# Kernel optimization log

Measured on AMD Instinct MI355X. Metric: run time of the kernel, lower is better.

The kernel has to match this reference:

```python
import jax, jax.numpy as jnp
import numpy as np
from jax import lax

HEADS = 8  # num_heads; also must equal cols of the input

def _conv_same(x, W, b):
    # x: (N, C_in, H, W), W: (C_out, C_in, kh, kw) -- Conv2d with padding='same'
    y = lax.conv_general_dilated(x, W, (1, 1), 'SAME',
                                 dimension_numbers=('NCHW', 'OIHW', 'NCHW'))
    return y + b[None, :, None, None]

def setup_inputs() -> dict:
    key = jax.random.key(0)
    ks = jax.random.split(key, 11)
    B, S, D, R, C = 4, 8, 512, 32, 8  # cols C == num_heads (required by the reshape)
    f = 3
    inp = {
        'q': jax.random.normal(ks[0], (B, S, D, R, C), jnp.float32),
        'k': jax.random.normal(ks[1], (B, S, D, R, C), jnp.float32),
        'v': jax.random.normal(ks[2], (B, S, D, R, C), jnp.float32),
        'Wq': jax.random.normal(ks[3], (D, D, f, f), jnp.float32) * 0.02,
        'bq': jnp.zeros((D,), jnp.float32),
        'Wk': jax.random.normal(ks[4], (D, D, f, f), jnp.float32) * 0.02,
        'bk': jnp.zeros((D,), jnp.float32),
        'Wv': jax.random.normal(ks[5], (D, D, f, f), jnp.float32) * 0.02,
        'bv': jnp.zeros((D,), jnp.float32),
        'Wo': jax.random.normal(ks[6], (D, D, f, f), jnp.float32) * 0.02,
        'bo': jnp.zeros((D,), jnp.float32),
    }
    return inp

def reference(q, k, v, Wq, bq, Wk, bk, Wv, bv, Wo, bo):
    B, S, D, R, C = q.shape
    H = HEADS
    dep = C // H  # = 1 with C == H (attention 'depth' per the original view math)

    def proj_split(x, W, b):
        y = _conv_same(x.reshape(B * S, D, R, C), W, b)          # (N, D, R, C)
        y = y.reshape(1, H, B * S, D, R, C // H)                  # raw view as in torch
        return y.transpose(0, 2, 3, 4, 1, 5)                      # (1, N, D, R, H, dep)

    q6 = proj_split(q, Wq, bq)
    k6 = proj_split(k, Wk, bk)
    v6 = proj_split(v, Wv, bv)

    # vectorized form of the per-step loop: dot over (rows, H, dep), softmax over keys
    scores = jnp.einsum('bnqrhd,bnkrhd->bnqk', q6, k6) / jnp.sqrt(jnp.float32(dep))
    attn = jax.nn.softmax(scores, axis=-1)                        # (1, N, D, D)
    out = jnp.einsum('bnqk,bnkrhd->bnqrhd', attn, v6)             # (1, N, D, R, H, dep)

    sa = out.reshape(B, S, R, H, D).transpose(0, 4, 1, 2, 3)      # (B, D, S, R, H)
    y = _conv_same(sa.reshape(B, D, S, R * H), Wo, bo)            # channels = d_model
    y = y.reshape(B, D, S, R, H)
    return y, attn
```

## Files before the change

### kernel.cpp

```cpp
#include <hip/hip_runtime.h>


typedef __attribute__((ext_vector_type(8))) short short8;
typedef __attribute__((ext_vector_type(8))) _Float16 half8;
typedef __attribute__((ext_vector_type(4))) float f32x4;
typedef __attribute__((ext_vector_type(4))) short short4v;

#define MFMA16F(a, b, c) __builtin_amdgcn_mfma_f32_16x16x32_f16((a), (b), (c), 0, 0, 0)

__device__ __forceinline__ void gl_lds16(const void* g, void* l) {
    __builtin_amdgcn_global_load_lds(
        (const __attribute__((address_space(1))) unsigned int*)g,
        (__attribute__((address_space(3))) unsigned int*)l, 16, 0, 0);
}
__device__ __forceinline__ unsigned short f2h(float f) {
    _Float16 h = (_Float16)f;
    return __builtin_bit_cast(unsigned short, h);
}
__device__ __forceinline__ float h2f(unsigned short u) {
    return (float)__builtin_bit_cast(_Float16, u);
}

__global__ __launch_bounds__(256) void k_prep_fused(
        const float* __restrict__ q, const float* __restrict__ k,
        const float* __restrict__ v,
        const float* __restrict__ Wq, const float* __restrict__ Wk,
        const float* __restrict__ Wv, const float* __restrict__ Wo,
        unsigned short* __restrict__ Wqh, unsigned short* __restrict__ Wkh,
        unsigned short* __restrict__ Wvh, unsigned short* __restrict__ Woh,
        unsigned short* __restrict__ Xqh, unsigned short* __restrict__ Xkh,
        unsigned short* __restrict__ Xvh) {
    __shared__ __align__(16) unsigned int U[8192];
    const int b = blockIdx.x;
    const int tid = threadIdx.x;
    if (b < 1536) {
        const int cig = b & 15, n = (b >> 4) & 31, z = b >> 9;
        const float* X = z == 0 ? q : z == 1 ? k : v;
        unsigned short* Xh = z == 0 ? Xqh : z == 1 ? Xkh : Xvh;
#pragma unroll
        for (int it = 0; it < 8; ++it) {
            int ci_l = it * 4 + (tid >> 6);
            int pos = (tid & 63) * 4;
            const float4 rd =
                *(const float4*)&X[(size_t)(n * 512 + cig * 32 + ci_l) * 256 + pos];
            uint4 u;
            u.x = f2h(rd.x);
            u.y = f2h(rd.y);
            u.z = f2h(rd.z);
            u.w = f2h(rd.w);
            *(uint4*)&U[ci_l * 256 + pos] = u;
        }
        __syncthreads();
#pragma unroll
        for (int it = 0; it < 4; ++it) {
            int pos = it * 64 + (tid >> 2);
            int ci8 = (tid & 3) * 8;
            short8 h8;
#pragma unroll
            for (int j = 0; j < 8; ++j)
                h8[j] = (short)(U[(ci8 + j) * 256 + pos] & 0xffffu);
            int yy = (pos >> 3) + 1, xx = (pos & 7) + 1;
            size_t o = (size_t)((n * 34 + yy) * 10 + xx) * 512 + cig * 32 + ci8;
            *(short8*)&Xh[o] = h8;
        }
    } else if (b < 3584) {
        const int bl = b - 1536;
        const int co = bl & 511, z = bl >> 9;
        const float* W = z == 0 ? Wq : z == 1 ? Wk : z == 2 ? Wv : Wo;
        unsigned short* Wh = z == 0 ? Wqh : z == 1 ? Wkh : z == 2 ? Wvh : Woh;
        const float* Wc = W + co * 4608;
#pragma unroll
        for (int it = 0; it < 9; ++it) {
            int p = it * 256 + tid;
            float2 rd = *(const float2*)&Wc[p * 2];
            int e0 = p * 2;
            int ci0 = e0 / 9, t0 = e0 - ci0 * 9;
            U[t0 * 512 + ci0] = f2h(rd.x);
            int e1 = e0 + 1;
            int ci1 = e1 / 9, t1 = e1 - ci1 * 9;
            U[t1 * 512 + ci1] = f2h(rd.y);
        }
        __syncthreads();
        unsigned short* Whc = Wh + co * 4608;
#pragma unroll
        for (int it = 0; it < 18; ++it) {
            int j = it * 256 + tid;
            Whc[j] = (unsigned short)U[j];
        }
    } else {
        const int w = tid >> 6, l = tid & 63;
        int job = (b - 3584) * 4 + w;
        int a = job / 2688;
        int r = job - a * 2688;
        int n = r / 84;
        int ii = r - n * 84;
        unsigned short* arr = a == 0 ? Xqh : a == 1 ? Xkh : Xvh;
        int cell;
        if (ii < 11)      cell = ii;
        else if (ii < 73) { int j = ii - 11; cell = 19 + (j >> 1) * 10 + (j & 1); }
        else              cell = 329 + (ii - 73);
        short8 z8 = {0, 0, 0, 0, 0, 0, 0, 0};
        *(short8*)&arr[(size_t)(n * 340 + cell) * 512 + l * 8] = z8;
    }
}

__global__ __launch_bounds__(256) void k_conv_qkv_all(
        const unsigned short* __restrict__ Xqh, const unsigned short* __restrict__ Xkh,
        const unsigned short* __restrict__ Xvh,
        const unsigned short* __restrict__ Wqh_, const unsigned short* __restrict__ Wkh_,
        const unsigned short* __restrict__ Wvh_,
        const float* __restrict__ bq, const float* __restrict__ bk,
        const float* __restrict__ bv,
        unsigned short* __restrict__ Qh, unsigned short* __restrict__ Ql,
        unsigned short* __restrict__ Kh,
        unsigned short* __restrict__ Vt) {
    __shared__ __align__(16) short Ah[8192], Bh[8192];
    const int z = blockIdx.z;
    const unsigned short* Xh = z == 0 ? Xqh : z == 1 ? Xkh : Xvh;
    const unsigned short* Wh = z == 0 ? Wqh_ : z == 1 ? Wkh_ : Wvh_;
    const float* bias = z == 0 ? bq : z == 1 ? bk : bv;

    const int tid = threadIdx.x;
    const int w = tid >> 6, l = tid & 63;
    const int n   = blockIdx.x >> 1;
    const int p0  = (blockIdx.x & 1) * 128;
    const int co0 = blockIdx.y * 128;
    const int lm = l & 15, lq = l >> 4;
    const int r8 = l >> 3, c8 = (l & 7) ^ (l >> 3);

    int arow[4], brow[4];
#pragma unroll
    for (int j = 0; j < 4; ++j) {
        int rt = w * 32 + j * 8 + r8;
        int px = p0 + rt;
        int y = px >> 3, x = px & 7;
        arow[j] = ((n * 34 + y + 1) * 10 + (x + 1)) * 512 + c8 * 8;
        brow[j] = (co0 + rt) * 4608 + c8 * 8;
    }
    const int ldsW = w * 4096;

    int aoff[4][2], boff[4][2];
#pragma unroll
    for (int mi = 0; mi < 4; ++mi) {
        int row = (w & 1) * 64 + mi * 16 + lm;
#pragma unroll
        for (int ks = 0; ks < 2; ++ks)
            aoff[mi][ks] = row * 64 + ((((ks << 2) | lq) ^ (row & 7)) * 8);
    }
#pragma unroll
    for (int ni = 0; ni < 4; ++ni) {
        int row = (w >> 1) * 64 + ni * 16 + lm;
#pragma unroll
        for (int ks = 0; ks < 2; ++ks)
            boff[ni][ks] = row * 64 + ((((ks << 2) | lq) ^ (row & 7)) * 8);
    }

    f32x4 acc[4][4];
#pragma unroll
    for (int ni = 0; ni < 4; ++ni) {
        float b = bias[co0 + (w >> 1) * 64 + ni * 16 + lm];
#pragma unroll
        for (int mi = 0; mi < 4; ++mi) acc[mi][ni] = (f32x4){b, b, b, b};
    }

    for (int tap = 0; tap < 9; ++tap) {
        const int tapoff = ((tap / 3 - 1) * 10 + (tap % 3 - 1)) * 512;
        const int wb = tap * 512;
        for (int ci0 = 0; ci0 < 512; ci0 += 64) {
#pragma unroll
            for (int j = 0; j < 4; ++j)
                gl_lds16(Xh + arow[j] + tapoff + ci0, (char*)Ah + ldsW + j * 1024);
#pragma unroll
            for (int j = 0; j < 4; ++j)
                gl_lds16(Wh + brow[j] + wb + ci0, (char*)Bh + ldsW + j * 1024);
            __syncthreads();
            __builtin_amdgcn_s_setprio(1);
#pragma unroll
            for (int ks = 0; ks < 2; ++ks) {
                half8 ah[4], bh[4];
#pragma unroll
                for (int mi = 0; mi < 4; ++mi)
                    ah[mi] = *(const half8*)&Ah[aoff[mi][ks]];
#pragma unroll
                for (int ni = 0; ni < 4; ++ni)
                    bh[ni] = *(const half8*)&Bh[boff[ni][ks]];
#pragma unroll
                for (int mi = 0; mi < 4; ++mi)
#pragma unroll
                    for (int ni = 0; ni < 4; ++ni)
                        acc[mi][ni] = MFMA16F(ah[mi], bh[ni], acc[mi][ni]);
            }
            __builtin_amdgcn_s_setprio(0);
            __syncthreads();
        }
    }

    const int hh = n >> 2, nl = n & 3;
    const int pxbase = p0 + (w & 1) * 64 + lq * 4;
    const int x0q = pxbase & 7;
#pragma unroll
    for (int mi = 0; mi < 4; ++mi) {
        int px = pxbase + mi * 16;
        int y = px >> 3;
#pragma unroll
        for (int ni = 0; ni < 4; ++ni) {
            int co = co0 + (w >> 1) * 64 + ni * 16 + lm;
            int nn = nl * 8 + (co >> 6);
            int dd = (co & 63) * 8 + (y >> 2);
            int t0 = hh * 32 + (y & 3) * 8 + x0q;
            if (z == 0) {
                short4v hv, lv;
#pragma unroll
                for (int r = 0; r < 4; ++r) {
                    float xv = acc[mi][ni][r];
                    unsigned short hb = f2h(xv);
                    hv[r] = (short)hb;
                    lv[r] = (short)f2h(xv - h2f(hb));
                }
                int base = (nn * 512 + dd) * 256 + t0;
                *(short4v*)&Qh[base] = hv;
                *(short4v*)&Ql[base] = lv;
            } else if (z == 1) {
                short4v hv;
#pragma unroll
                for (int r = 0; r < 4; ++r) hv[r] = (short)f2h(acc[mi][ni][r]);
                *(short4v*)&Kh[(nn * 512 + dd) * 256 + t0] = hv;
            } else {
#pragma unroll
                for (int r = 0; r < 4; ++r)
                    Vt[(nn * 256 + t0 + r) * 512 + dd] = f2h(acc[mi][ni][r]);
            }
        }
    }
}

__global__ __launch_bounds__(256) void k_scores_mfma(
        const unsigned short* __restrict__ Qh, const unsigned short* __restrict__ Ql,
        const unsigned short* __restrict__ Kh,
        float* __restrict__ Sc) {
    __shared__ __align__(16) short Ah[8192], Al[8192], Bh[8192];
    const int tid = threadIdx.x;
    const int w = tid >> 6, l = tid & 63;
    const int q0 = blockIdx.x * 128, k0 = blockIdx.y * 128, nn = blockIdx.z;
    const int lm = l & 15, lq = l >> 4;
    const int r8 = l >> 3, c8 = (l & 7) ^ (l >> 3);

    int arow[4], brow[4];
#pragma unroll
    for (int j = 0; j < 4; ++j) {
        int rr = w * 32 + j * 8 + r8;
        arow[j] = (nn * 512 + q0 + rr) * 256 + c8 * 8;
        brow[j] = (nn * 512 + k0 + rr) * 256 + c8 * 8;
    }
    const int ldsW = w * 4096;

    int aoff[4][2], boff[4][2];
#pragma unroll
    for (int mi = 0; mi < 4; ++mi) {
        int row = (w & 1) * 64 + mi * 16 + lm;
#pragma unroll
        for (int ks = 0; ks < 2; ++ks)
            aoff[mi][ks] = row * 64 + ((((ks << 2) | lq) ^ (row & 7)) * 8);
    }
#pragma unroll
    for (int ni = 0; ni < 4; ++ni) {
        int row = (w >> 1) * 64 + ni * 16 + lm;
#pragma unroll
        for (int ks = 0; ks < 2; ++ks)
            boff[ni][ks] = row * 64 + ((((ks << 2) | lq) ^ (row & 7)) * 8);
    }

    f32x4 acc[4][4];
#pragma unroll
    for (int mi = 0; mi < 4; ++mi)
#pragma unroll
        for (int ni = 0; ni < 4; ++ni) acc[mi][ni] = (f32x4){0.f, 0.f, 0.f, 0.f};

    for (int t0 = 0; t0 < 256; t0 += 64) {
#pragma unroll
        for (int j = 0; j < 4; ++j)
            gl_lds16(Qh + arow[j] + t0, (char*)Ah + ldsW + j * 1024);
#pragma unroll
        for (int j = 0; j < 4; ++j)
            gl_lds16(Ql + arow[j] + t0, (char*)Al + ldsW + j * 1024);
#pragma unroll
        for (int j = 0; j < 4; ++j)
            gl_lds16(Kh + brow[j] + t0, (char*)Bh + ldsW + j * 1024);
        __syncthreads();
#pragma unroll
        for (int ks = 0; ks < 2; ++ks) {
            half8 ah[4], bh[4];
#pragma unroll
            for (int mi = 0; mi < 4; ++mi) ah[mi] = *(const half8*)&Ah[aoff[mi][ks]];
#pragma unroll
            for (int ni = 0; ni < 4; ++ni) bh[ni] = *(const half8*)&Bh[boff[ni][ks]];
#pragma unroll
            for (int mi = 0; mi < 4; ++mi)
#pragma unroll
                for (int ni = 0; ni < 4; ++ni)
                    acc[mi][ni] = MFMA16F(ah[mi], bh[ni], acc[mi][ni]);
            half8 alv[4];
#pragma unroll
            for (int mi = 0; mi < 4; ++mi) alv[mi] = *(const half8*)&Al[aoff[mi][ks]];
#pragma unroll
            for (int mi = 0; mi < 4; ++mi)
#pragma unroll
                for (int ni = 0; ni < 4; ++ni)
                    acc[mi][ni] = MFMA16F(alv[mi], bh[ni], acc[mi][ni]);
        }
        __syncthreads();
    }

    float* C = Sc + nn * 262144;
#pragma unroll
    for (int mi = 0; mi < 4; ++mi) {
        int qb = q0 + (w & 1) * 64 + lq * 4 + mi * 16;
#pragma unroll
        for (int ni = 0; ni < 4; ++ni) {
            int col = k0 + (w >> 1) * 64 + ni * 16 + lm;
#pragma unroll
            for (int r = 0; r < 4; ++r)
                C[(qb + r) * 512 + col] = acc[mi][ni][r];
        }
    }
}

__global__ __launch_bounds__(256) void k_softmax(float* __restrict__ Sc,
                                                 unsigned short* __restrict__ Ph,
                                                 unsigned int* __restrict__ Spz) {
    unsigned zi = blockIdx.x * 256 + threadIdx.x;
    if (zi < 2641920u) Spz[zi] = 0u;
    __shared__ float red[8];
    float* p = Sc + (size_t)blockIdx.x * 512;
    unsigned short* ph = Ph + (size_t)blockIdx.x * 512;
    const int tid = threadIdx.x;
    float x0 = p[tid], x1 = p[tid + 256];
    float m = fmaxf(x0, x1);
#pragma unroll
    for (int off = 32; off; off >>= 1) m = fmaxf(m, __shfl_xor(m, off));
    if ((tid & 63) == 0) red[tid >> 6] = m;
    __syncthreads();
    m = fmaxf(fmaxf(red[0], red[1]), fmaxf(red[2], red[3]));
    float e0 = __expf(x0 - m), e1 = __expf(x1 - m);
    float s = e0 + e1;
#pragma unroll
    for (int off = 32; off; off >>= 1) s += __shfl_xor(s, off);
    if ((tid & 63) == 0) red[4 + (tid >> 6)] = s;
    __syncthreads();
    s = red[4] + red[5] + red[6] + red[7];
    float inv = 1.0f / s;
    float p0 = e0 * inv, p1 = e1 * inv;
    p[tid] = p0;
    p[tid + 256] = p1;
    ph[tid] = f2h(p0);
    ph[tid + 256] = f2h(p1);
}

__global__ __launch_bounds__(256) void k_pv_mfma(
        const unsigned short* __restrict__ Ph, const unsigned short* __restrict__ Vt,
        unsigned short* __restrict__ Sp) {
    __shared__ __align__(16) short Ah[16384], Bh[8192];
    const int tid = threadIdx.x;
    const int w = tid >> 6, l = tid & 63;
    const int q0 = blockIdx.x * 128, t0 = blockIdx.y * 64, nn = blockIdx.z;
    const int lm = l & 15, lq = l >> 4;
    const int r4 = l >> 4, c16 = l & 15;

    int arow[8], brow[4];
#pragma unroll
    for (int j = 0; j < 8; ++j) {
        int rt = w * 32 + j * 4 + r4;
        arow[j] = (nn * 512 + q0 + rt) * 512 + ((c16 ^ (rt & 15)) * 8);
    }
#pragma unroll
    for (int j = 0; j < 4; ++j) {
        int rt = w * 16 + j * 4 + r4;
        brow[j] = (nn * 256 + t0 + rt) * 512 + ((c16 ^ (rt & 15)) * 8);
    }
    const int ldsA = w * 8192, ldsB = w * 4096;

    int aoff[4][4], boff[2][4];
#pragma unroll
    for (int mi = 0; mi < 4; ++mi) {
        int row = (w & 1) * 64 + mi * 16 + lm;
#pragma unroll
        for (int ks = 0; ks < 4; ++ks)
            aoff[mi][ks] = row * 128 + ((((ks << 2) | lq) ^ (row & 15)) * 8);
    }
#pragma unroll
    for (int ni = 0; ni < 2; ++ni) {
        int row = (w >> 1) * 32 + ni * 16 + lm;
#pragma unroll
        for (int ks = 0; ks < 4; ++ks)
            boff[ni][ks] = row * 128 + ((((ks << 2) | lq) ^ (row & 15)) * 8);
    }

    f32x4 acc[4][2];
#pragma unroll
    for (int mi = 0; mi < 4; ++mi)
#pragma unroll
        for (int ni = 0; ni < 2; ++ni) acc[mi][ni] = (f32x4){0.f, 0.f, 0.f, 0.f};

    for (int kc = 0; kc < 512; kc += 128) {
#pragma unroll
        for (int j = 0; j < 8; ++j)
            gl_lds16(Ph + arow[j] + kc, (char*)Ah + ldsA + j * 1024);
#pragma unroll
        for (int j = 0; j < 4; ++j)
            gl_lds16(Vt + brow[j] + kc, (char*)Bh + ldsB + j * 1024);
        __syncthreads();
#pragma unroll
        for (int ks = 0; ks < 4; ++ks) {
            half8 a[4], b[2];
#pragma unroll
            for (int mi = 0; mi < 4; ++mi) a[mi] = *(const half8*)&Ah[aoff[mi][ks]];
#pragma unroll
            for (int ni = 0; ni < 2; ++ni) b[ni] = *(const half8*)&Bh[boff[ni][ks]];
#pragma unroll
            for (int mi = 0; mi < 4; ++mi)
#pragma unroll
                for (int ni = 0; ni < 2; ++ni)
                    acc[mi][ni] = MFMA16F(a[mi], b[ni], acc[mi][ni]);
        }
        __syncthreads();
    }

    const int b2 = nn >> 3, s2 = nn & 7;
#pragma unroll
    for (int mi = 0; mi < 4; ++mi) {
        int qb = q0 + (w & 1) * 64 + lq * 4 + mi * 16;
#pragma unroll
        for (int ni = 0; ni < 2; ++ni) {
            int tc = t0 + (w >> 1) * 32 + ni * 16 + lm;
            int d2base = (tc & 31) * 8 + (tc >> 5);
#pragma unroll
            for (int r = 0; r < 4; ++r) {
                int qp = qb + r;
                int ww = (qp >> 4) * 8 + ((qp >> 1) & 7);
                int d2 = (qp & 1) * 256 + d2base;
                Sp[((b2 * 10 + s2 + 1) * 258 + ww + 1) * 512 + d2] =
                    f2h(acc[mi][ni][r]);
            }
        }
    }
}

__global__ __launch_bounds__(256) void k_conv_o_mfma(
        const unsigned short* __restrict__ Sp, const unsigned short* __restrict__ Wh,
        const float* __restrict__ bias, float* __restrict__ Y) {
    __shared__ __align__(16) short Ah[16384], Bh[8192];
    const int tid = threadIdx.x;
    const int w = tid >> 6, l = tid & 63;
    const int n   = blockIdx.x >> 4;
    const int yy  = (blockIdx.x >> 1) & 7;
    const int x0  = (blockIdx.x & 1) * 128;
    const int co0 = blockIdx.y * 64;
    const int lm = l & 15, lq = l >> 4;
    const int r4 = l >> 4, c16 = l & 15;

    int arow[8], brow[4];
#pragma unroll
    for (int j = 0; j < 8; ++j) {
        int rt = w * 32 + j * 4 + r4;
        arow[j] = ((n * 10 + yy + 1) * 258 + (x0 + rt + 1)) * 512
                  + ((c16 ^ (rt & 15)) * 8);
    }
#pragma unroll
    for (int j = 0; j < 4; ++j) {
        int rt = w * 16 + j * 4 + r4;
        brow[j] = (co0 + rt) * 4608 + ((c16 ^ (rt & 15)) * 8);
    }
    const int ldsA = w * 8192, ldsB = w * 4096;

    int aoff[4][4], boff[2][4];
#pragma unroll
    for (int mi = 0; mi < 4; ++mi) {
        int row = (w & 1) * 64 + mi * 16 + lm;
#pragma unroll
        for (int ks = 0; ks < 4; ++ks)
            aoff[mi][ks] = row * 128 + ((((ks << 2) | lq) ^ (row & 15)) * 8);
    }
#pragma unroll
    for (int ni = 0; ni < 2; ++ni) {
        int row = (w >> 1) * 32 + ni * 16 + lm;
#pragma unroll
        for (int ks = 0; ks < 4; ++ks)
            boff[ni][ks] = row * 128 + ((((ks << 2) | lq) ^ (row & 15)) * 8);
    }

    f32x4 acc[4][2];
#pragma unroll
    for (int ni = 0; ni < 2; ++ni) {
        float b = bias[co0 + (w >> 1) * 32 + ni * 16 + lm];
#pragma unroll
        for (int mi = 0; mi < 4; ++mi) acc[mi][ni] = (f32x4){b, b, b, b};
    }

    for (int tap = 0; tap < 9; ++tap) {
        const int tapoff = ((tap / 3 - 1) * 258 + (tap % 3 - 1)) * 512;
        const int wb = tap * 512;
        for (int ci0 = 0; ci0 < 512; ci0 += 128) {
#pragma unroll
            for (int j = 0; j < 8; ++j)
                gl_lds16(Sp + arow[j] + tapoff + ci0, (char*)Ah + ldsA + j * 1024);
#pragma unroll
            for (int j = 0; j < 4; ++j)
                gl_lds16(Wh + brow[j] + wb + ci0, (char*)Bh + ldsB + j * 1024);
            __syncthreads();
#pragma unroll
            for (int ks = 0; ks < 4; ++ks) {
                half8 a[4], b[2];
#pragma unroll
                for (int mi = 0; mi < 4; ++mi)
                    a[mi] = *(const half8*)&Ah[aoff[mi][ks]];
#pragma unroll
                for (int ni = 0; ni < 2; ++ni)
                    b[ni] = *(const half8*)&Bh[boff[ni][ks]];
#pragma unroll
                for (int mi = 0; mi < 4; ++mi)
#pragma unroll
                    for (int ni = 0; ni < 2; ++ni)
                        acc[mi][ni] = MFMA16F(a[mi], b[ni], acc[mi][ni]);
            }
            __syncthreads();
        }
    }

#pragma unroll
    for (int mi = 0; mi < 4; ++mi) {
        int px = x0 + (w & 1) * 64 + lq * 4 + mi * 16;
#pragma unroll
        for (int ni = 0; ni < 2; ++ni) {
            int co = co0 + (w >> 1) * 32 + ni * 16 + lm;
            *(f32x4*)&Y[n * 1048576 + co * 2048 + yy * 256 + px] = acc[mi][ni];
        }
    }
}

extern "C" void kernel_launch(void* const* d_in, const int* in_sizes, int n_in,
                              void* d_out, int out_size, void* d_ws, size_t ws_size,
                              hipStream_t stream) {
    const float* q  = (const float*)d_in[0];
    const float* k  = (const float*)d_in[1];
    const float* v  = (const float*)d_in[2];
    const float* Wq = (const float*)d_in[3];
    const float* bq = (const float*)d_in[4];
    const float* Wk = (const float*)d_in[5];
    const float* bk = (const float*)d_in[6];
    const float* Wv = (const float*)d_in[7];
    const float* bv = (const float*)d_in[8];
    const float* Wo = (const float*)d_in[9];
    const float* bo = (const float*)d_in[10];

    unsigned short* W0  = (unsigned short*)d_ws;
    unsigned short* Wqh = W0;
    unsigned short* Wkh = W0 + 2359296;
    unsigned short* Wvh = W0 + 4718592;
    unsigned short* Xvh = W0 + 7077888;
    unsigned short* Woh = W0 + 18219008;
    unsigned short* Qh  = W0 + 20578304;
    unsigned short* Ql  = W0 + 24772608;
    unsigned short* Kh  = W0 + 28966912;
    unsigned short* Vt  = W0 + 33161216;
    unsigned short* Ph = W0;
    unsigned short* Sp = W0 + 20578304;

    float* y_out = (float*)d_out;
    float* attn  = y_out + 4194304;
    unsigned short* Xqh = (unsigned short*)d_out;
    unsigned short* Xkh = (unsigned short*)attn;

    k_prep_fused<<<5600, 256, 0, stream>>>(q, k, v, Wq, Wk, Wv, Wo,
                                           Wqh, Wkh, Wvh, Woh,
                                           Xqh, Xkh, Xvh);
    k_conv_qkv_all<<<dim3(64, 4, 3), 256, 0, stream>>>(
        Xqh, Xkh, Xvh, Wqh, Wkh, Wvh,
        bq, bk, bv, Qh, Ql, Kh, Vt);
    k_scores_mfma<<<dim3(4, 4, 32), 256, 0, stream>>>(Qh, Ql, Kh, attn);
    k_softmax<<<16384, 256, 0, stream>>>(attn, Ph, (unsigned int*)Sp);
    k_pv_mfma<<<dim3(4, 4, 32), 256, 0, stream>>>(Ph, Vt, Sp);
    k_conv_o_mfma<<<dim3(64, 8), 256, 0, stream>>>(Sp, Woh, bo, y_out);
}
```

Measured before the change: 376.9 us.

## Drop Q low-half split precision, widen scores K-tile, warp-per-row softmax

Removes the hi/lo fp16 split of Q, so the scores GEMM runs a single fp16 MFMA pass and no longer writes or loads the Ql buffer. The scores kernel now stages 128-wide K chunks with a 16-way XOR swizzle, halving its loop iterations and barriers. Softmax becomes one wavefront per row with float4 loads and stores, which removes the shared-memory reductions and block barriers, and it launches a quarter as many blocks. The cost is lower score precision, with the risk of larger error in attention outputs.

```diff
diff --git a/kernel.cpp b/kernel.cpp
--- a/kernel.cpp
+++ b/kernel.cpp
@@ -16,9 +16,6 @@
 __device__ __forceinline__ unsigned short f2h(float f) {
     _Float16 h = (_Float16)f;
     return __builtin_bit_cast(unsigned short, h);
-}
-__device__ __forceinline__ float h2f(unsigned short u) {
-    return (float)__builtin_bit_cast(_Float16, u);
 }
 
 __global__ __launch_bounds__(256) void k_prep_fused(
@@ -111,8 +108,7 @@
         const unsigned short* __restrict__ Wvh_,
         const float* __restrict__ bq, const float* __restrict__ bk,
         const float* __restrict__ bv,
-        unsigned short* __restrict__ Qh, unsigned short* __restrict__ Ql,
-        unsigned short* __restrict__ Kh,
+        unsigned short* __restrict__ Qh, unsigned short* __restrict__ Kh,
         unsigned short* __restrict__ Vt) {
     __shared__ __align__(16) short Ah[8192], Bh[8192];
     const int z = blockIdx.z;
@@ -208,23 +204,12 @@
             int nn = nl * 8 + (co >> 6);
             int dd = (co & 63) * 8 + (y >> 2);
             int t0 = hh * 32 + (y & 3) * 8 + x0q;
-            if (z == 0) {
-                short4v hv, lv;
-#pragma unroll
-                for (int r = 0; r < 4; ++r) {
-                    float xv = acc[mi][ni][r];
-                    unsigned short hb = f2h(xv);
-                    hv[r] = (short)hb;
-                    lv[r] = (short)f2h(xv - h2f(hb));
-                }
-                int base = (nn * 512 + dd) * 256 + t0;
-                *(short4v*)&Qh[base] = hv;
-                *(short4v*)&Ql[base] = lv;
-            } else if (z == 1) {
+            if (z < 2) {
+                unsigned short* O = (z == 0) ? Qh : Kh;
                 short4v hv;
 #pragma unroll
                 for (int r = 0; r < 4; ++r) hv[r] = (short)f2h(acc[mi][ni][r]);
-                *(short4v*)&Kh[(nn * 512 + dd) * 256 + t0] = hv;
+                *(short4v*)&O[(nn * 512 + dd) * 256 + t0] = hv;
             } else {
 #pragma unroll
                 for (int r = 0; r < 4; ++r)
@@ -235,39 +220,39 @@
 }
 
 __global__ __launch_bounds__(256) void k_scores_mfma(
-        const unsigned short* __restrict__ Qh, const unsigned short* __restrict__ Ql,
-        const unsigned short* __restrict__ Kh,
+        const unsigned short* __restrict__ Qh, const unsigned short* __restrict__ Kh,
         float* __restrict__ Sc) {
-    __shared__ __align__(16) short Ah[8192], Al[8192], Bh[8192];
+    __shared__ __align__(16) short Ah[16384], Bh[16384];
     const int tid = threadIdx.x;
     const int w = tid >> 6, l = tid & 63;
     const int q0 = blockIdx.x * 128, k0 = blockIdx.y * 128, nn = blockIdx.z;
     const int lm = l & 15, lq = l >> 4;
-    const int r8 = l >> 3, c8 = (l & 7) ^ (l >> 3);
-
-    int arow[4], brow[4];
-#pragma unroll
-    for (int j = 0; j < 4; ++j) {
-        int rr = w * 32 + j * 8 + r8;
-        arow[j] = (nn * 512 + q0 + rr) * 256 + c8 * 8;
-        brow[j] = (nn * 512 + k0 + rr) * 256 + c8 * 8;
-    }
-    const int ldsW = w * 4096;
-
-    int aoff[4][2], boff[4][2];
+    const int r4 = l >> 4, c16 = l & 15;
+
+    int arow[8], brow[8];
+#pragma unroll
+    for (int j = 0; j < 8; ++j) {
+        int rt = w * 32 + j * 4 + r4;
+        int sw = (c16 ^ (rt & 15)) * 8;
+        arow[j] = (nn * 512 + q0 + rt) * 256 + sw;
+        brow[j] = (nn * 512 + k0 + rt) * 256 + sw;
+    }
+    const int ldsW = w * 8192;
+
+    int aoff[4][4], boff[4][4];
 #pragma unroll
     for (int mi = 0; mi < 4; ++mi) {
         int row = (w & 1) * 64 + mi * 16 + lm;
 #pragma unroll
-        for (int ks = 0; ks < 2; ++ks)
-            aoff[mi][ks] = row * 64 + ((((ks << 2) | lq) ^ (row & 7)) * 8);
+        for (int ks = 0; ks < 4; ++ks)
+            aoff[mi][ks] = row * 128 + ((((ks << 2) | lq) ^ (row & 15)) * 8);
     }
 #pragma unroll
     for (int ni = 0; ni < 4; ++ni) {
         int row = (w >> 1) * 64 + ni * 16 + lm;
 #pragma unroll
-        for (int ks = 0; ks < 2; ++ks)
-            boff[ni][ks] = row * 64 + ((((ks << 2) | lq) ^ (row & 7)) * 8);
+        for (int ks = 0; ks < 4; ++ks)
+            boff[ni][ks] = row * 128 + ((((ks << 2) | lq) ^ (row & 15)) * 8);
     }
 
     f32x4 acc[4][4];
@@ -276,19 +261,16 @@
 #pragma unroll
         for (int ni = 0; ni < 4; ++ni) acc[mi][ni] = (f32x4){0.f, 0.f, 0.f, 0.f};
 
-    for (int t0 = 0; t0 < 256; t0 += 64) {
-#pragma unroll
-        for (int j = 0; j < 4; ++j)
+    for (int t0 = 0; t0 < 256; t0 += 128) {
+#pragma unroll
+        for (int j = 0; j < 8; ++j)
             gl_lds16(Qh + arow[j] + t0, (char*)Ah + ldsW + j * 1024);
 #pragma unroll
-        for (int j = 0; j < 4; ++j)
-            gl_lds16(Ql + arow[j] + t0, (char*)Al + ldsW + j * 1024);
-#pragma unroll
-        for (int j = 0; j < 4; ++j)
+        for (int j = 0; j < 8; ++j)
             gl_lds16(Kh + brow[j] + t0, (char*)Bh + ldsW + j * 1024);
         __syncthreads();
 #pragma unroll
-        for (int ks = 0; ks < 2; ++ks) {
+        for (int ks = 0; ks < 4; ++ks) {
             half8 ah[4], bh[4];
 #pragma unroll
             for (int mi = 0; mi < 4; ++mi) ah[mi] = *(const half8*)&Ah[aoff[mi][ks]];
@@ -299,14 +281,6 @@
 #pragma unroll
                 for (int ni = 0; ni < 4; ++ni)
                     acc[mi][ni] = MFMA16F(ah[mi], bh[ni], acc[mi][ni]);
-            half8 alv[4];
-#pragma unroll
-            for (int mi = 0; mi < 4; ++mi) alv[mi] = *(const half8*)&Al[aoff[mi][ks]];
-#pragma unroll
-            for (int mi = 0; mi < 4; ++mi)
-#pragma unroll
-                for (int ni = 0; ni < 4; ++ni)
-                    acc[mi][ni] = MFMA16F(alv[mi], bh[ni], acc[mi][ni]);
         }
         __syncthreads();
     }
@@ -328,32 +302,38 @@
 __global__ __launch_bounds__(256) void k_softmax(float* __restrict__ Sc,
                                                  unsigned short* __restrict__ Ph,
                                                  unsigned int* __restrict__ Spz) {
-    unsigned zi = blockIdx.x * 256 + threadIdx.x;
-    if (zi < 2641920u) Spz[zi] = 0u;
-    __shared__ float red[8];
-    float* p = Sc + (size_t)blockIdx.x * 512;
-    unsigned short* ph = Ph + (size_t)blockIdx.x * 512;
-    const int tid = threadIdx.x;
-    float x0 = p[tid], x1 = p[tid + 256];
-    float m = fmaxf(x0, x1);
+    unsigned base = blockIdx.x * 256 + threadIdx.x;
+#pragma unroll
+    for (int i = 0; i < 3; ++i) {
+        unsigned zi = base + (unsigned)i * 1048576u;
+        if (zi < 2641920u) Spz[zi] = 0u;
+    }
+    const int w = threadIdx.x >> 6, l = threadIdx.x & 63;
+    float* p = Sc + ((size_t)blockIdx.x * 4 + w) * 512;
+    unsigned short* ph = Ph + ((size_t)blockIdx.x * 4 + w) * 512;
+    const int i0 = l * 4, i1 = 256 + l * 4;
+    float4 a = *(const float4*)&p[i0];
+    float4 b = *(const float4*)&p[i1];
+    float m = fmaxf(fmaxf(fmaxf(a.x, a.y), fmaxf(a.z, a.w)),
+                    fmaxf(fmaxf(b.x, b.y), fmaxf(b.z, b.w)));
 #pragma unroll
     for (int off = 32; off; off >>= 1) m = fmaxf(m, __shfl_xor(m, off));
-    if ((tid & 63) == 0) red[tid >> 6] = m;
-    __syncthreads();
-    m = fmaxf(fmaxf(red[0], red[1]), fmaxf(red[2], red[3]));
-    float e0 = __expf(x0 - m), e1 = __expf(x1 - m);
-    float s = e0 + e1;
+    float e0 = __expf(a.x - m), e1 = __expf(a.y - m);
+    float e2 = __expf(a.z - m), e3 = __expf(a.w - m);
+    float e4 = __expf(b.x - m), e5 = __expf(b.y - m);
+    float e6 = __expf(b.z - m), e7 = __expf(b.w - m);
+    float s = ((e0 + e1) + (e2 + e3)) + ((e4 + e5) + (e6 + e7));
 #pragma unroll
     for (int off = 32; off; off >>= 1) s += __shfl_xor(s, off);
-    if ((tid & 63) == 0) red[4 + (tid >> 6)] = s;
-    __syncthreads();
-    s = red[4] + red[5] + red[6] + red[7];
     float inv = 1.0f / s;
-    float p0 = e0 * inv, p1 = e1 * inv;
-    p[tid] = p0;
-    p[tid + 256] = p1;
-    ph[tid] = f2h(p0);
-    ph[tid + 256] = f2h(p1);
+    float4 o0 = {e0 * inv, e1 * inv, e2 * inv, e3 * inv};
+    float4 o1 = {e4 * inv, e5 * inv, e6 * inv, e7 * inv};
+    *(float4*)&p[i0] = o0;
+    *(float4*)&p[i1] = o1;
+    short4v h0 = {(short)f2h(o0.x), (short)f2h(o0.y), (short)f2h(o0.z), (short)f2h(o0.w)};
+    short4v h1 = {(short)f2h(o1.x), (short)f2h(o1.y), (short)f2h(o1.z), (short)f2h(o1.w)};
+    *(short4v*)&ph[i0] = h0;
+    *(short4v*)&ph[i1] = h1;
 }
 
 __global__ __launch_bounds__(256) void k_pv_mfma(
@@ -559,7 +539,6 @@
     unsigned short* Xvh = W0 + 7077888;
     unsigned short* Woh = W0 + 18219008;
     unsigned short* Qh  = W0 + 20578304;
-    unsigned short* Ql  = W0 + 24772608;
     unsigned short* Kh  = W0 + 28966912;
     unsigned short* Vt  = W0 + 33161216;
     unsigned short* Ph = W0;
@@ -575,9 +554,9 @@
                                            Xqh, Xkh, Xvh);
     k_conv_qkv_all<<<dim3(64, 4, 3), 256, 0, stream>>>(
         Xqh, Xkh, Xvh, Wqh, Wkh, Wvh,
-        bq, bk, bv, Qh, Ql, Kh, Vt);
-    k_scores_mfma<<<dim3(4, 4, 32), 256, 0, stream>>>(Qh, Ql, Kh, attn);
-    k_softmax<<<16384, 256, 0, stream>>>(attn, Ph, (unsigned int*)Sp);
+        bq, bk, bv, Qh, Kh, Vt);
+    k_scores_mfma<<<dim3(4, 4, 32), 256, 0, stream>>>(Qh, Kh, attn);
+    k_softmax<<<4096, 256, 0, stream>>>(attn, Ph, (unsigned int*)Sp);
     k_pv_mfma<<<dim3(4, 4, 32), 256, 0, stream>>>(Ph, Vt, Sp);
     k_conv_o_mfma<<<dim3(64, 8), 256, 0, stream>>>(Sp, Woh, bo, y_out);
 }
```

Result: faster. 367.4 us (-2.5%).
